# Kernel optimization log

Measured on AMD Instinct MI355X. Metric: run time of the kernel, lower is better.

The kernel has to match this reference:

```python
import jax, jax.numpy as jnp
import numpy as np

B, S, E, H = 8, 512, 768, 12
EPS = 1e-5  # torch LayerNorm default

def setup_inputs() -> dict:
    key = jax.random.key(0)
    ks = jax.random.split(key, 6)
    s = 1.0 / np.sqrt(E)
    return {
        "x": jax.random.normal(ks[0], (B, S, E), jnp.float32),
        "atten_pad_mask": jax.random.randint(ks[1], (B, 1, S), 0, 2, jnp.int32),
        # per-head shared q/k/v projection weights, stacked: [H, E_in, E_out]
        "Wh": jax.random.normal(ks[2], (H, E, E), jnp.float32) * s,
        "bh": jax.random.normal(ks[3], (H, E), jnp.float32) * s,
        # output projection: [H*E, E]
        "Wo": jax.random.normal(ks[4], (H * E, E), jnp.float32) * (1.0 / np.sqrt(H * E)),
        "bo": jnp.zeros((E,), jnp.float32),
        "gamma": jnp.ones((E,), jnp.float32),
        "beta": jnp.zeros((E,), jnp.float32),
    }

def reference(x, atten_pad_mask, Wh, bh, Wo, bo, gamma, beta):
    # Each head applies ONE shared linear to q=k=v=x (faithful to SelfAttention).
    p = jnp.einsum('bse,heo->bhso', x, Wh) + bh[None, :, None, :]  # [B,H,S,E]
    scores = jnp.einsum('bhqe,bhke->bhqk', p, p) / np.sqrt(E)      # [B,H,S,S]
    # masked_fill(mask == 1, -inf); mask [B,1,S] -> broadcast [B,1,1,S]
    scores = jnp.where(atten_pad_mask[:, None, :, :] == 1, -jnp.inf, scores)
    attn = jax.nn.softmax(scores, axis=-1)
    o = jnp.einsum('bhqk,bhke->bhqe', attn, p)                     # [B,H,S,E]
    cat = o.transpose(0, 2, 1, 3).reshape(B, S, H * E)             # concat heads
    y = cat @ Wo + bo                                              # [B,S,E]
    mu = jnp.mean(y, axis=-1, keepdims=True)
    var = jnp.var(y, axis=-1, keepdims=True)
    return (y - mu) / jnp.sqrt(var + EPS) * gamma + beta
```

## Files before the change

kernel.cpp:

```cpp
#include <hip/hip_runtime.h>
#include <hip/hip_bf16.h>
#include <math.h>

#define B_ 8
#define S_ 512
#define E_ 768
#define H_ 12
#define HE_ (H_ * E_)
#define KSPLIT 6
#define KCHUNK (HE_ / KSPLIT)

typedef __attribute__((ext_vector_type(4))) short bf16x4;
typedef __attribute__((ext_vector_type(8))) short bf16x8;
typedef __attribute__((ext_vector_type(4))) float f32x4;
typedef __attribute__((ext_vector_type(16))) float f32x16;
typedef __attribute__((ext_vector_type(4))) int i32x4;

__device__ inline void gload_lds16(const void* g, void* l) {
  __builtin_amdgcn_global_load_lds(
      (const __attribute__((address_space(1))) unsigned int*)g,
      (__attribute__((address_space(3))) unsigned int*)l, 16, 0, 0);
}

__device__ inline float bf2f(short u) {
  union { float f; unsigned int i; } c;
  c.i = ((unsigned int)(unsigned short)u) << 16;
  return c.f;
}
__device__ inline short f2bf(float f) {
  __hip_bfloat16 h = __float2bfloat16(f);
  return *reinterpret_cast<short*>(&h);
}

__global__ __launch_bounds__(256) void cvt_v(const float* __restrict__ in,
                                             short* __restrict__ out) {
  const long i = ((long)blockIdx.x * 256 + threadIdx.x) * 4;
  float4 v = *reinterpret_cast<const float4*>(in + i);
  bf16x4 o;
  o[0] = f2bf(v.x); o[1] = f2bf(v.y); o[2] = f2bf(v.z); o[3] = f2bf(v.w);
  *reinterpret_cast<bf16x4*>(out + i) = o;
}

template <typename T, int VW>
__global__ __launch_bounds__(256) void transpose_v(const T* __restrict__ in, long inz,
                                                   short* __restrict__ out, long outz,
                                                   int R, int C) {
  __shared__ float t[64][65];
  in += (long)blockIdx.z * inz;
  out += (long)blockIdx.z * outz;
  const int bc = blockIdx.x * 64, br = blockIdx.y * 64;
  const int tid = threadIdx.x;
  constexpr int CPR = 64 / VW;
  constexpr int NP1 = 64 * CPR / 256;
#pragma unroll
  for (int ps = 0; ps < NP1; ++ps) {
    int q = tid + ps * 256;
    int r = q / CPR, c0 = (q % CPR) * VW;
    const T* src = in + (long)(br + r) * C + bc + c0;
    if constexpr (VW == 4) {
      float4 v = *reinterpret_cast<const float4*>(src);
      t[r][c0] = v.x; t[r][c0 + 1] = v.y; t[r][c0 + 2] = v.z; t[r][c0 + 3] = v.w;
    } else {
      bf16x8 v = *reinterpret_cast<const bf16x8*>(src);
#pragma unroll
      for (int j = 0; j < 8; ++j) t[r][c0 + j] = bf2f(v[j]);
    }
  }
  __syncthreads();
#pragma unroll
  for (int ps = 0; ps < 2; ++ps) {
    int q = tid + ps * 256;
    int e = q >> 3, s0 = (q & 7) * 8;
    bf16x8 o;
#pragma unroll
    for (int j = 0; j < 8; ++j) o[j] = f2bf(t[s0 + j][e]);
    *reinterpret_cast<bf16x8*>(out + (long)(bc + e) * R + br + s0) = o;
  }
}

template <bool OUT_BF16, bool ADD_BIAS>
__global__ __launch_bounds__(256) void gemm_bt(
    const __hip_bfloat16* __restrict__ A, long As1, long As2, int lda,
    const __hip_bfloat16* __restrict__ BT, long Bs1, long Bs2, int ldb,
    void* __restrict__ Cv, long Cs1, long Cs2, int ldc,
    const float* __restrict__ bias, long biasS2, int zmod, int K, float scale,
    int nx, int ny) {
  constexpr int BM = 128, BN = 128, BK = 64;
  __shared__ __align__(16) __hip_bfloat16 sA[BM * BK];
  __shared__ __align__(16) __hip_bfloat16 sB[BN * BK];
  const int nwg = gridDim.x;
  const int cpx = nwg >> 3;
  const int id = blockIdx.x;
  const int w = (id & 7) * cpx + (id >> 3);
  const int bz = w / (nx * ny);
  const int rem = w - bz * nx * ny;
  const int by = rem / nx;
  const int bx = rem - by * nx;

  const int tid = threadIdx.x;
  const int wave = tid >> 6, lane = tid & 63;
  const int r32 = lane & 31, g2 = lane >> 5;
  const int zb = bz / zmod, zh = bz % zmod;
  A += (long)zb * As1 + (long)zh * As2;
  BT += (long)zb * Bs1 + (long)zh * Bs2;
  const int bm = by * BM, bn = bx * BN;
  const int wm = (wave >> 1) * 64, wn = (wave & 1) * 64;
  const int swz = (r32 & 7) << 3;
  f32x16 acc[2][2] = {};
  const int e0 = tid * 8;

  for (int k0 = 0; k0 < K; k0 += BK) {
#pragma unroll
    for (int p = 0; p < 4; ++p) {
      int ee = p * 2048 + e0;
      int row = ee >> 6;
      int col = (ee & 63) ^ ((row & 7) << 3);
      gload_lds16(A + (long)(bm + row) * lda + (k0 + col), (char*)sA + ee * 2);
      gload_lds16(BT + (long)(bn + row) * ldb + (k0 + col), (char*)sB + ee * 2);
    }
    __syncthreads();
#pragma unroll
    for (int ks = 0; ks < 4; ++ks) {
      bf16x8 aw[2], bw[2];
#pragma unroll
      for (int ti = 0; ti < 2; ++ti) {
        int row = wm + ti * 32 + r32;
        int c = (ks * 16 + g2 * 8) ^ swz;
        aw[ti] = *(const bf16x8*)(const void*)(sA + row * BK + c);
      }
#pragma unroll
      for (int tj = 0; tj < 2; ++tj) {
        int row = wn + tj * 32 + r32;
        int c = (ks * 16 + g2 * 8) ^ swz;
        bw[tj] = *(const bf16x8*)(const void*)(sB + row * BK + c);
      }
#pragma unroll
      for (int ti = 0; ti < 2; ++ti)
#pragma unroll
        for (int tj = 0; tj < 2; ++tj)
          acc[ti][tj] =
              __builtin_amdgcn_mfma_f32_32x32x16_bf16(aw[ti], bw[tj], acc[ti][tj], 0, 0, 0);
    }
    __syncthreads();
  }

  float* Cf = (float*)Cv;
  __hip_bfloat16* Cb = (__hip_bfloat16*)Cv;
  const long cbase = (long)zb * Cs1 + (long)zh * Cs2;
#pragma unroll
  for (int ti = 0; ti < 2; ++ti)
#pragma unroll
    for (int tj = 0; tj < 2; ++tj) {
      const int colv = bn + wn + tj * 32 + r32;
      const float bv = ADD_BIAS ? bias[(long)zh * biasS2 + colv] : 0.0f;
#pragma unroll
      for (int r = 0; r < 16; ++r) {
        int rowv = bm + wm + ti * 32 + (r & 3) + 8 * (r >> 2) + 4 * g2;
        float v = acc[ti][tj][r] * scale + bv;
        long off = cbase + (long)rowv * ldc + colv;
        if (OUT_BF16)
          Cb[off] = __float2bfloat16(v);
        else
          Cf[off] = v;
      }
    }
}

__global__ __launch_bounds__(256) void softmax_v(__hip_bfloat16* __restrict__ scores,
                                                 const int* __restrict__ mask) {
  const int wave = threadIdx.x >> 6, lane = threadIdx.x & 63;
  const long row = (long)blockIdx.x * 4 + wave;
  const int b = (int)(row / ((long)H_ * S_));
  short* sp = (short*)scores + row * S_ + lane * 8;
  bf16x8 sv = *reinterpret_cast<const bf16x8*>(sp);
  const int* mrow = mask + (long)b * S_ + lane * 8;
  i32x4 m0 = *reinterpret_cast<const i32x4*>(mrow);
  i32x4 m1 = *reinterpret_cast<const i32x4*>(mrow + 4);
  float v[8];
#pragma unroll
  for (int j = 0; j < 8; ++j) v[j] = bf2f(sv[j]);
  if (m0[0] == 1) v[0] = -INFINITY;
  if (m0[1] == 1) v[1] = -INFINITY;
  if (m0[2] == 1) v[2] = -INFINITY;
  if (m0[3] == 1) v[3] = -INFINITY;
  if (m1[0] == 1) v[4] = -INFINITY;
  if (m1[1] == 1) v[5] = -INFINITY;
  if (m1[2] == 1) v[6] = -INFINITY;
  if (m1[3] == 1) v[7] = -INFINITY;
  float mx = v[0];
#pragma unroll
  for (int j = 1; j < 8; ++j) mx = fmaxf(mx, v[j]);
#pragma unroll
  for (int o = 32; o; o >>= 1) mx = fmaxf(mx, __shfl_xor(mx, o));
  float e[8], s = 0.0f;
#pragma unroll
  for (int j = 0; j < 8; ++j) {
    e[j] = expf(v[j] - mx);
    s += e[j];
  }
#pragma unroll
  for (int o = 32; o; o >>= 1) s += __shfl_xor(s, o);
  const float inv = 1.0f / s;
  bf16x8 o8;
#pragma unroll
  for (int j = 0; j < 8; ++j) o8[j] = f2bf(e[j] * inv);
  *reinterpret_cast<bf16x8*>(sp) = o8;
}

__global__ __launch_bounds__(192) void ln_v(const __hip_bfloat16* __restrict__ yp,
                                            const float* __restrict__ bo,
                                            const float* __restrict__ gamma,
                                            const float* __restrict__ beta,
                                            float* __restrict__ out) {
  const long nY = (long)B_ * S_ * E_;
  const long base = (long)blockIdx.x * E_;
  const int t = threadIdx.x;
  const int c0 = t * 4;
  float a[4];
  {
    float4 bv = *reinterpret_cast<const float4*>(bo + c0);
    a[0] = bv.x; a[1] = bv.y; a[2] = bv.z; a[3] = bv.w;
  }
#pragma unroll
  for (int k = 0; k < KSPLIT; ++k) {
    bf16x4 v = *reinterpret_cast<const bf16x4*>((const short*)yp + k * nY + base + c0);
#pragma unroll
    for (int j = 0; j < 4; ++j) a[j] += bf2f(v[j]);
  }
  float s = a[0] + a[1] + a[2] + a[3];
  float ss = a[0] * a[0] + a[1] * a[1] + a[2] * a[2] + a[3] * a[3];
#pragma unroll
  for (int o = 32; o; o >>= 1) {
    s += __shfl_xor(s, o);
    ss += __shfl_xor(ss, o);
  }
  __shared__ float r1[3], r2[3];
  const int wave = t >> 6, lane = t & 63;
  if (lane == 0) { r1[wave] = s; r2[wave] = ss; }
  __syncthreads();
  s = r1[0] + r1[1] + r1[2];
  ss = r2[0] + r2[1] + r2[2];
  const float mu = s * (1.0f / E_);
  const float var = ss * (1.0f / E_) - mu * mu;
  const float rstd = rsqrtf(var + 1e-5f);
  float4 g = *reinterpret_cast<const float4*>(gamma + c0);
  float4 bt = *reinterpret_cast<const float4*>(beta + c0);
  float4 o4;
  o4.x = (a[0] - mu) * rstd * g.x + bt.x;
  o4.y = (a[1] - mu) * rstd * g.y + bt.y;
  o4.z = (a[2] - mu) * rstd * g.z + bt.z;
  o4.w = (a[3] - mu) * rstd * g.w + bt.w;
  *reinterpret_cast<float4*>(out + base + c0) = o4;
}

extern "C" void kernel_launch(void* const* d_in, const int* in_sizes, int n_in,
                              void* d_out, int out_size, void* d_ws, size_t ws_size,
                              hipStream_t stream) {
  const float* x = (const float*)d_in[0];
  const int* mask = (const int*)d_in[1];
  const float* Wh = (const float*)d_in[2];
  const float* bh = (const float*)d_in[3];
  const float* Wo = (const float*)d_in[4];
  const float* bo = (const float*)d_in[5];
  const float* gamma = (const float*)d_in[6];
  const float* beta = (const float*)d_in[7];
  float* out = (float*)d_out;

  const size_t nX = (size_t)B_ * S_ * E_;
  const size_t nP = (size_t)B_ * H_ * S_ * E_;
  const size_t nSc = (size_t)B_ * H_ * S_ * S_;
  char* base = (char*)d_ws;
  __hip_bfloat16* p = (__hip_bfloat16*)base;
  __hip_bfloat16* cat = p;
  char* RB = base + nP * 2;
  __hip_bfloat16* pT = (__hip_bfloat16*)RB;
  __hip_bfloat16* ypart = (__hip_bfloat16*)RB;
  char* RC = RB + nP * 2;
  __hip_bfloat16* xb = (__hip_bfloat16*)RC;
  __hip_bfloat16* WhT = (__hip_bfloat16*)(RC + nX * 2);
  __hip_bfloat16* scores = (__hip_bfloat16*)RC;
  char* RD = RC + nSc * 2;
  __hip_bfloat16* WoT = (__hip_bfloat16*)RD;

  dim3 t256(256);
  const float inv_sqrtE = 1.0f / sqrtf((float)E_);

  cvt_v<<<dim3(nX / 1024), t256, 0, stream>>>(x, (short*)xb);
  transpose_v<float, 4><<<dim3(12, 12, 12), t256, 0, stream>>>(
      Wh, (long)E_ * E_, (short*)WhT, (long)E_ * E_, E_, E_);
  transpose_v<float, 4><<<dim3(12, 144, 1), t256, 0, stream>>>(
      Wo, 0, (short*)WoT, 0, HE_, E_);
  gemm_bt<true, true><<<dim3(6 * 4 * 96), t256, 0, stream>>>(
      xb, (long)S_ * E_, 0, E_, WhT, 0, (long)E_ * E_, E_, p, (long)H_ * S_ * E_,
      (long)S_ * E_, E_, bh, E_, H_, E_, 1.0f, 6, 4);
  transpose_v<short, 8><<<dim3(12, 8, 96), t256, 0, stream>>>(
      (const short*)p, (long)S_ * E_, (short*)pT, (long)S_ * E_, S_, E_);
  gemm_bt<true, false><<<dim3(4 * 4 * 96), t256, 0, stream>>>(
      p, (long)H_ * S_ * E_, (long)S_ * E_, E_, p, (long)H_ * S_ * E_, (long)S_ * E_, E_,
      scores, (long)H_ * S_ * S_, (long)S_ * S_, S_, nullptr, 0, H_, E_, inv_sqrtE, 4, 4);
  softmax_v<<<dim3(12288), t256, 0, stream>>>(scores, mask);
  gemm_bt<true, false><<<dim3(6 * 4 * 96), t256, 0, stream>>>(
      scores, (long)H_ * S_ * S_, (long)S_ * S_, S_, pT, (long)H_ * E_ * S_, (long)E_ * S_,
      S_, cat, (long)S_ * HE_, (long)E_, HE_, nullptr, 0, H_, S_, 1.0f, 6, 4);
  gemm_bt<true, false><<<dim3(6 * 32 * KSPLIT), t256, 0, stream>>>(
      cat, 0, KCHUNK, HE_, WoT, 0, KCHUNK, HE_, ypart, 0, (long)B_ * S_ * E_, E_,
      nullptr, 0, KSPLIT, KCHUNK, 1.0f, 6, 32);
  ln_v<<<dim3(B_ * S_), dim3(192), 0, stream>>>(ypart, bo, gamma, beta, out);
}
```

Baseline: 306.9 us.

## Compact unmasked keys to skip masked columns in attention GEMMs

A new scan kernel builds, per batch, a list of unmasked key indices and their count padded to 64. The scores GEMM gathers only those key rows and skips column tiles past the padded count. Softmax masks by count instead of reading the mask. The P·V GEMM shrinks its K loop to the padded count and reads a gathered, transposed copy of p. This removes the work spent on keys that softmax would zero anyway, at the cost of an extra scan launch and indirect row loads in the GEMM.

```diff
diff --git a/kernel.cpp b/kernel.cpp
--- a/kernel.cpp
+++ b/kernel.cpp
@@ -12,9 +12,7 @@
 
 typedef __attribute__((ext_vector_type(4))) short bf16x4;
 typedef __attribute__((ext_vector_type(8))) short bf16x8;
-typedef __attribute__((ext_vector_type(4))) float f32x4;
 typedef __attribute__((ext_vector_type(16))) float f32x16;
-typedef __attribute__((ext_vector_type(4))) int i32x4;
 
 __device__ inline void gload_lds16(const void* g, void* l) {
   __builtin_amdgcn_global_load_lds(
@@ -39,6 +37,33 @@
   bf16x4 o;
   o[0] = f2bf(v.x); o[1] = f2bf(v.y); o[2] = f2bf(v.z); o[3] = f2bf(v.w);
   *reinterpret_cast<bf16x4*>(out + i) = o;
+}
+
+__global__ __launch_bounds__(512) void mask_scan(const int* __restrict__ mask,
+                                                 int* __restrict__ idx,
+                                                 int* __restrict__ cntp) {
+  const int b = blockIdx.x;
+  const int t = threadIdx.x;
+  const int wave = t >> 6, lane = t & 63;
+  const bool keep = (mask[b * S_ + t] == 0);
+  unsigned long long bal = __ballot(keep);
+  const int wprefix = __popcll(bal & ((1ull << lane) - 1ull));
+  __shared__ int wt[8];
+  if (lane == 0) wt[wave] = __popcll(bal);
+  idx[b * S_ + t] = 0;
+  __syncthreads();
+  int off = 0, total = 0;
+#pragma unroll
+  for (int i = 0; i < 8; ++i) {
+    off += (i < wave) ? wt[i] : 0;
+    total += wt[i];
+  }
+  if (keep) idx[b * S_ + off + wprefix] = t;
+  if (t == 0) {
+    cntp[2 * b] = total;
+    int pad = (total + 63) & ~63;
+    cntp[2 * b + 1] = pad > S_ ? S_ : pad;
+  }
 }
 
 template <typename T, int VW>
@@ -78,13 +103,46 @@
   }
 }
 
-template <bool OUT_BF16, bool ADD_BIAS>
+__global__ __launch_bounds__(256) void transpose_gather(const short* __restrict__ p,
+                                                        const int* __restrict__ gidx,
+                                                        const int* __restrict__ cntp,
+                                                        short* __restrict__ out) {
+  const int z = blockIdx.z, b = z / H_;
+  const int br = blockIdx.y * 64;
+  if (br >= cntp[2 * b + 1]) return;
+  __shared__ float t[64][65];
+  const short* in = p + (long)z * S_ * E_;
+  short* o = out + (long)z * S_ * E_;
+  const int bc = blockIdx.x * 64;
+  const int tid = threadIdx.x;
+#pragma unroll
+  for (int ps = 0; ps < 2; ++ps) {
+    int q = tid + ps * 256;
+    int r = q >> 3, c0 = (q & 7) * 8;
+    int srow = gidx[b * S_ + br + r];
+    bf16x8 v = *reinterpret_cast<const bf16x8*>(in + (long)srow * E_ + bc + c0);
+#pragma unroll
+    for (int j = 0; j < 8; ++j) t[r][c0 + j] = bf2f(v[j]);
+  }
+  __syncthreads();
+#pragma unroll
+  for (int ps = 0; ps < 2; ++ps) {
+    int q = tid + ps * 256;
+    int e = q >> 3, s0 = (q & 7) * 8;
+    bf16x8 o8;
+#pragma unroll
+    for (int j = 0; j < 8; ++j) o8[j] = f2bf(t[s0 + j][e]);
+    *reinterpret_cast<bf16x8*>(o + (long)(bc + e) * S_ + br + s0) = o8;
+  }
+}
+
+template <bool OUT_BF16, bool ADD_BIAS, bool GATHER_B, bool K_FROM_CNT>
 __global__ __launch_bounds__(256) void gemm_bt(
     const __hip_bfloat16* __restrict__ A, long As1, long As2, int lda,
     const __hip_bfloat16* __restrict__ BT, long Bs1, long Bs2, int ldb,
     void* __restrict__ Cv, long Cs1, long Cs2, int ldc,
     const float* __restrict__ bias, long biasS2, int zmod, int K, float scale,
-    int nx, int ny) {
+    int nx, int ny, const int* __restrict__ gidx, const int* __restrict__ cntp) {
   constexpr int BM = 128, BN = 128, BK = 64;
   __shared__ __align__(16) __hip_bfloat16 sA[BM * BK];
   __shared__ __align__(16) __hip_bfloat16 sB[BN * BK];
@@ -101,22 +159,33 @@
   const int wave = tid >> 6, lane = tid & 63;
   const int r32 = lane & 31, g2 = lane >> 5;
   const int zb = bz / zmod, zh = bz % zmod;
+  const int bm = by * BM, bn = bx * BN;
+  if (GATHER_B && bn >= cntp[2 * zb + 1]) return;
+  int Keff = K;
+  if (K_FROM_CNT) Keff = cntp[2 * zb + 1];
   A += (long)zb * As1 + (long)zh * As2;
   BT += (long)zb * Bs1 + (long)zh * Bs2;
-  const int bm = by * BM, bn = bx * BN;
   const int wm = (wave >> 1) * 64, wn = (wave & 1) * 64;
   const int swz = (r32 & 7) << 3;
   f32x16 acc[2][2] = {};
   const int e0 = tid * 8;
 
-  for (int k0 = 0; k0 < K; k0 += BK) {
+  int colp[4], rowp[4], growB[4];
+#pragma unroll
+  for (int p = 0; p < 4; ++p) {
+    int ee = p * 2048 + e0;
+    int row = ee >> 6;
+    rowp[p] = row;
+    colp[p] = (ee & 63) ^ ((row & 7) << 3);
+    growB[p] = GATHER_B ? gidx[zb * S_ + bn + row] : (bn + row);
+  }
+
+  for (int k0 = 0; k0 < Keff; k0 += BK) {
 #pragma unroll
     for (int p = 0; p < 4; ++p) {
       int ee = p * 2048 + e0;
-      int row = ee >> 6;
-      int col = (ee & 63) ^ ((row & 7) << 3);
-      gload_lds16(A + (long)(bm + row) * lda + (k0 + col), (char*)sA + ee * 2);
-      gload_lds16(BT + (long)(bn + row) * ldb + (k0 + col), (char*)sB + ee * 2);
+      gload_lds16(A + (long)(bm + rowp[p]) * lda + (k0 + colp[p]), (char*)sA + ee * 2);
+      gload_lds16(BT + (long)growB[p] * ldb + (k0 + colp[p]), (char*)sB + ee * 2);
     }
     __syncthreads();
 #pragma unroll
@@ -167,26 +236,17 @@
 }
 
 __global__ __launch_bounds__(256) void softmax_v(__hip_bfloat16* __restrict__ scores,
-                                                 const int* __restrict__ mask) {
+                                                 const int* __restrict__ cntp) {
   const int wave = threadIdx.x >> 6, lane = threadIdx.x & 63;
   const long row = (long)blockIdx.x * 4 + wave;
   const int b = (int)(row / ((long)H_ * S_));
+  const int cnt = cntp[2 * b];
   short* sp = (short*)scores + row * S_ + lane * 8;
   bf16x8 sv = *reinterpret_cast<const bf16x8*>(sp);
-  const int* mrow = mask + (long)b * S_ + lane * 8;
-  i32x4 m0 = *reinterpret_cast<const i32x4*>(mrow);
-  i32x4 m1 = *reinterpret_cast<const i32x4*>(mrow + 4);
+  const int j0 = lane * 8;
   float v[8];
 #pragma unroll
-  for (int j = 0; j < 8; ++j) v[j] = bf2f(sv[j]);
-  if (m0[0] == 1) v[0] = -INFINITY;
-  if (m0[1] == 1) v[1] = -INFINITY;
-  if (m0[2] == 1) v[2] = -INFINITY;
-  if (m0[3] == 1) v[3] = -INFINITY;
-  if (m1[0] == 1) v[4] = -INFINITY;
-  if (m1[1] == 1) v[5] = -INFINITY;
-  if (m1[2] == 1) v[6] = -INFINITY;
-  if (m1[3] == 1) v[7] = -INFINITY;
+  for (int j = 0; j < 8; ++j) v[j] = (j0 + j < cnt) ? bf2f(sv[j]) : -INFINITY;
   float mx = v[0];
 #pragma unroll
   for (int j = 1; j < 8; ++j) mx = fmaxf(mx, v[j]);
@@ -267,13 +327,14 @@
   float* out = (float*)d_out;
 
   const size_t nX = (size_t)B_ * S_ * E_;
+  const size_t nWh = (size_t)H_ * E_ * E_;
   const size_t nP = (size_t)B_ * H_ * S_ * E_;
   const size_t nSc = (size_t)B_ * H_ * S_ * S_;
   char* base = (char*)d_ws;
   __hip_bfloat16* p = (__hip_bfloat16*)base;
   __hip_bfloat16* cat = p;
   char* RB = base + nP * 2;
-  __hip_bfloat16* pT = (__hip_bfloat16*)RB;
+  __hip_bfloat16* pcT = (__hip_bfloat16*)RB;
   __hip_bfloat16* ypart = (__hip_bfloat16*)RB;
   char* RC = RB + nP * 2;
   __hip_bfloat16* xb = (__hip_bfloat16*)RC;
@@ -281,29 +342,34 @@
   __hip_bfloat16* scores = (__hip_bfloat16*)RC;
   char* RD = RC + nSc * 2;
   __hip_bfloat16* WoT = (__hip_bfloat16*)RD;
+  int* idx = (int*)(RD + nWh * 2);
+  int* cntp = idx + B_ * S_;
 
   dim3 t256(256);
   const float inv_sqrtE = 1.0f / sqrtf((float)E_);
 
+  mask_scan<<<dim3(B_), dim3(512), 0, stream>>>(mask, idx, cntp);
   cvt_v<<<dim3(nX / 1024), t256, 0, stream>>>(x, (short*)xb);
   transpose_v<float, 4><<<dim3(12, 12, 12), t256, 0, stream>>>(
       Wh, (long)E_ * E_, (short*)WhT, (long)E_ * E_, E_, E_);
   transpose_v<float, 4><<<dim3(12, 144, 1), t256, 0, stream>>>(
       Wo, 0, (short*)WoT, 0, HE_, E_);
-  gemm_bt<true, true><<<dim3(6 * 4 * 96), t256, 0, stream>>>(
+  gemm_bt<true, true, false, false><<<dim3(6 * 4 * 96), t256, 0, stream>>>(
       xb, (long)S_ * E_, 0, E_, WhT, 0, (long)E_ * E_, E_, p, (long)H_ * S_ * E_,
-      (long)S_ * E_, E_, bh, E_, H_, E_, 1.0f, 6, 4);
-  transpose_v<short, 8><<<dim3(12, 8, 96), t256, 0, stream>>>(
-      (const short*)p, (long)S_ * E_, (short*)pT, (long)S_ * E_, S_, E_);
-  gemm_bt<true, false><<<dim3(4 * 4 * 96), t256, 0, stream>>>(
+      (long)S_ * E_, E_, bh, E_, H_, E_, 1.0f, 6, 4, nullptr, nullptr);
+  gemm_bt<true, false, true, false><<<dim3(4 * 4 * 96), t256, 0, stream>>>(
       p, (long)H_ * S_ * E_, (long)S_ * E_, E_, p, (long)H_ * S_ * E_, (long)S_ * E_, E_,
-      scores, (long)H_ * S_ * S_, (long)S_ * S_, S_, nullptr, 0, H_, E_, inv_sqrtE, 4, 4);
-  softmax_v<<<dim3(12288), t256, 0, stream>>>(scores, mask);
-  gemm_bt<true, false><<<dim3(6 * 4 * 96), t256, 0, stream>>>(
-      scores, (long)H_ * S_ * S_, (long)S_ * S_, S_, pT, (long)H_ * E_ * S_, (long)E_ * S_,
-      S_, cat, (long)S_ * HE_, (long)E_, HE_, nullptr, 0, H_, S_, 1.0f, 6, 4);
-  gemm_bt<true, false><<<dim3(6 * 32 * KSPLIT), t256, 0, stream>>>(
+      scores, (long)H_ * S_ * S_, (long)S_ * S_, S_, nullptr, 0, H_, E_, inv_sqrtE, 4, 4,
+      idx, cntp);
+  softmax_v<<<dim3(12288), t256, 0, stream>>>(scores, cntp);
+  transpose_gather<<<dim3(12, 8, 96), t256, 0, stream>>>((const short*)p, idx, cntp,
+                                                         (short*)pcT);
+  gemm_bt<true, false, false, true><<<dim3(6 * 4 * 96), t256, 0, stream>>>(
+      scores, (long)H_ * S_ * S_, (long)S_ * S_, S_, pcT, (long)H_ * E_ * S_,
+      (long)E_ * S_, S_, cat, (long)S_ * HE_, (long)E_, HE_, nullptr, 0, H_, S_, 1.0f,
+      6, 4, nullptr, cntp);
+  gemm_bt<true, false, false, false><<<dim3(6 * 32 * KSPLIT), t256, 0, stream>>>(
       cat, 0, KCHUNK, HE_, WoT, 0, KCHUNK, HE_, ypart, 0, (long)B_ * S_ * E_, E_,
-      nullptr, 0, KSPLIT, KCHUNK, 1.0f, 6, 32);
+      nullptr, 0, KSPLIT, KCHUNK, 1.0f, 6, 32, nullptr, nullptr);
   ln_v<<<dim3(B_ * S_), dim3(192), 0, stream>>>(ypart, bo, gamma, beta, out);
 }
```

After: 278.8 us, median of 3. 1.1x faster.
